# Kernel optimization log

Hardware: AMD Instinct MI355X
Metric: run time of the kernel (lower is better)

The kernel has to match this reference:

```python
import jax, jax.numpy as jnp
import numpy as np

GH, GW, H = 9, 9, 128
EPS = 1e-5


def _ln(v, g, b):
    mu = v.mean(-1, keepdims=True)
    var = ((v - mu) ** 2).mean(-1, keepdims=True)
    return (v - mu) * jax.lax.rsqrt(var + EPS) * g + b


def _bn(v, g, b):
    # BatchNorm1d in training mode: batch statistics, biased variance
    mu = v.mean(0)
    var = ((v - mu) ** 2).mean(0)
    return (v - mu) * jax.lax.rsqrt(var + EPS) * g + b


def _forward(x, h_ext, c_ext, h_grid0, c_grid0, Wh, bh, Wc, bc,
             lnh_g, lnh_b, lnc_g, lnc_b, W_ih, b_ih, W_hh, b_hh,
             fc1_W, fc1_b, bn1_g, bn1_b, fc2_W, fc2_b, bn2_g, bn2_b,
             fc3_W, fc3_b, bno_g, bno_b):
    B = x.shape[0]
    zeros = jnp.zeros((B, H), x.dtype)
    h_cur = [[None] * GW for _ in range(GH)]
    c_cur = [[None] * GW for _ in range(GH)]
    for i in range(GH):
        for j in range(GW):
            k = i * GW + j
            h_prev, c_prev = h_grid0[i, j], c_grid0[i, j]  # [B, H]
            if i == 0 and j == 0:
                h_left, c_left = h_ext, c_ext
            elif j > 0:
                h_left, c_left = h_cur[i][j - 1], c_cur[i][j - 1]
            else:
                h_left, c_left = zeros, zeros
            if i > 0:
                h_up, c_up = h_cur[i - 1][j], c_cur[i - 1][j]
            else:
                h_up, c_up = zeros, zeros
            comb_h = jnp.concatenate([h_left, h_up, h_prev], axis=1)  # [B, 3H]
            comb_c = jnp.concatenate([c_left, c_up, c_prev], axis=1)
            ph = _ln(comb_h @ Wh[k].T + bh[k], lnh_g[k], lnh_b[k])  # dropout is identity (eval)
            pc = _ln(comb_c @ Wc[k].T + bc[k], lnc_g[k], lnc_b[k])
            xin = x[:, i, j][:, None]  # [B, 1]
            gates = xin @ W_ih[k].T + b_ih[k] + ph @ W_hh[k].T + b_hh[k]  # [B, 4H]
            ig, fg, gg, og = jnp.split(gates, 4, axis=1)
            c_new = jax.nn.sigmoid(fg) * pc + jax.nn.sigmoid(ig) * jnp.tanh(gg)
            h_new = jax.nn.sigmoid(og) * jnp.tanh(c_new)
            h_cur[i][j], c_cur[i][j] = h_new, c_new
    final_h = h_cur[-1][-1] + h_ext
    final_c = c_cur[-1][-1] + c_ext
    z = jnp.concatenate([final_h, final_c], axis=1)  # [B, 2H]
    z = jax.nn.relu(_bn(z @ fc1_W.T + fc1_b, bn1_g, bn1_b))
    z = jax.nn.relu(_bn(z @ fc2_W.T + fc2_b, bn2_g, bn2_b))
    z = z @ fc3_W.T + fc3_b
    return jax.nn.sigmoid(_bn(z, bno_g, bno_b))


def setup_inputs() -> dict:
    key = jax.random.key(0)
    ks = jax.random.split(key, 16)
    B, OUT = 4096, 1
    N = GH * GW
    s = 0.05
    f32 = jnp.float32
    return {
        "x": jax.random.normal(ks[0], (B, GH, GW), f32),
        "h_ext": jax.random.normal(ks[1], (B, H), f32),
        "c_ext": jax.random.normal(ks[2], (B, H), f32),
        "h_grid0": jnp.zeros((GH, GW, B, H), f32),
        "c_grid0": jnp.zeros((GH, GW, B, H), f32),
        "Wh": jax.random.normal(ks[3], (N, H, 3 * H), f32) * s,
        "bh": jnp.zeros((N, H), f32),
        "Wc": jax.random.normal(ks[4], (N, H, 3 * H), f32) * s,
        "bc": jnp.zeros((N, H), f32),
        "lnh_g": jnp.ones((N, H), f32),
        "lnh_b": jnp.zeros((N, H), f32),
        "lnc_g": jnp.ones((N, H), f32),
        "lnc_b": jnp.zeros((N, H), f32),
        "W_ih": jax.random.normal(ks[5], (N, 4 * H, 1), f32) * s,
        "b_ih": jnp.zeros((N, 4 * H), f32),
        "W_hh": jax.random.normal(ks[6], (N, 4 * H, H), f32) * s,
        "b_hh": jnp.zeros((N, 4 * H), f32),
        "fc1_W": jax.random.normal(ks[7], (256, 2 * H), f32) * s,
        "fc1_b": jnp.zeros((256,), f32),
        "bn1_g": jnp.ones((256,), f32),
        "bn1_b": jnp.zeros((256,), f32),
        "fc2_W": jax.random.normal(ks[8], (128, 256), f32) * s,
        "fc2_b": jnp.zeros((128,), f32),
        "bn2_g": jnp.ones((128,), f32),
        "bn2_b": jnp.zeros((128,), f32),
        "fc3_W": jax.random.normal(ks[9], (OUT, 128), f32) * s,
        "fc3_b": jnp.zeros((OUT,), f32),
        "bno_g": jnp.ones((OUT,), f32),
        "bno_b": jnp.zeros((OUT,), f32),
    }


def reference(x, h_ext, c_ext, h_grid0, c_grid0, Wh, bh, Wc, bc,
              lnh_g, lnh_b, lnc_g, lnc_b, W_ih, b_ih, W_hh, b_hh,
              fc1_W, fc1_b, bn1_g, bn1_b, fc2_W, fc2_b, bn2_g, bn2_b,
              fc3_W, fc3_b, bno_g, bno_b):
    return _forward(x, h_ext, c_ext, h_grid0, c_grid0, Wh, bh, Wc, bc,
                    lnh_g, lnh_b, lnc_g, lnc_b, W_ih, b_ih, W_hh, b_hh,
                    fc1_W, fc1_b, bn1_g, bn1_b, fc2_W, fc2_b, bn2_g, bn2_b,
                    fc3_W, fc3_b, bno_g, bno_b)
```

## Files before the change

### kernel.cpp

```cpp
#include <hip/hip_runtime.h>
#include <math.h>

#define HH      128
#define GHN     9
#define GWN     9
#define BATCH   4096
#define NCELL   81
#define MSAMP   16
#define THREADS 512
#define NBLK    (BATCH / MSAMP)
#define EPSF    1e-5f

typedef __attribute__((ext_vector_type(8))) short  bf8;
typedef __attribute__((ext_vector_type(4))) short  short4v;
typedef __attribute__((ext_vector_type(4))) float  f32x4;

#define MFMA(a, b, c) __builtin_amdgcn_mfma_f32_16x16x32_bf16(a, b, c, 0, 0, 0)

__device__ __forceinline__ float rcp_fast(float x) { return __builtin_amdgcn_rcpf(x); }
__device__ __forceinline__ float rsq_fast(float x) { return __builtin_amdgcn_rsqf(x); }
__device__ __forceinline__ float sigm(float x)     { return rcp_fast(1.f + __expf(-x)); }
__device__ __forceinline__ float tanh_fast(float x) {
    float ax = fabsf(x);
    float t  = __expf(-2.f * ax);
    float r  = (1.f - t) * rcp_fast(1.f + t);
    return (x < 0.f) ? -r : r;
}
__device__ __forceinline__ short f2bf(float f) {
    unsigned u = __float_as_uint(f);
    u = (u + 0x7FFFu + ((u >> 16) & 1u)) >> 16;
    return (short)u;
}
__device__ __forceinline__ float bf2f(short h) {
    return __uint_as_float(((unsigned)(unsigned short)h) << 16);
}
__device__ __forceinline__ void split_bf(float f, short& hi, short& lo) {
    hi = f2bf(f);
    lo = f2bf(f - bf2f(hi));
}
__device__ __forceinline__ void store_frag4(short* hiA, short* loA, int idx, float4 v) {
    short4v h, l; short a, b;
    split_bf(v.x, a, b); h.x = a; l.x = b;
    split_bf(v.y, a, b); h.y = a; l.y = b;
    split_bf(v.z, a, b); h.z = a; l.z = b;
    split_bf(v.w, a, b); h.w = a; l.w = b;
    *(short4v*)&hiA[idx] = h;
    *(short4v*)&loA[idx] = l;
}
__device__ __forceinline__ int frag4_idx(int k, int m) {
    return (k >> 5) * 512 + ((((k & 31) >> 3) << 4) | m) * 8 + (k & 7);
}

__global__ __launch_bounds__(256)
void k_buildw(const float* __restrict__ Wh, const float* __restrict__ Wc,
              const float* __restrict__ Whh,
              short* __restrict__ whB_hi, short* __restrict__ whB_lo,
              short* __restrict__ wcB_hi, short* __restrict__ wcB_lo,
              short* __restrict__ whhB_hi, short* __restrict__ whhB_lo)
{
    __shared__ float lw[32 * 384];
    const int u  = threadIdx.x;
    const int kc = blockIdx.x / 24;
    const int c  = blockIdx.x % 24;

    if (c < 8) {
        const int mat = c >> 2;
        const int p   = c & 3;
        const float* src = (mat ? Wc : Wh) + ((size_t)kc * 128 + 32 * p) * 384;
        #pragma unroll
        for (int it = 0; it < 12; ++it)
            ((float4*)lw)[it * 256 + u] = ((const float4*)src)[it * 256 + u];
        __syncthreads();
        short* Dhi = mat ? wcB_hi : whB_hi;
        short* Dlo = mat ? wcB_lo : whB_lo;
        #pragma unroll
        for (int it = 0; it < 6; ++it) {
            const int wd = it * 256 + u;
            const int tt = wd / 768;
            const int rm = wd - tt * 768;
            const int s  = rm >> 6;
            const int l  = rm & 63;
            const int rl = tt * 16 + (l & 15);
            const int kk = s * 32 + (l >> 4) * 8;
            const float* pr = &lw[rl * 384 + kk];
            const float4 v0 = *(const float4*)pr;
            const float4 v1 = *(const float4*)(pr + 4);
            const size_t dst = (((size_t)kc * 8 + (2 * p + tt)) * 12 + s) * 512 + l * 8;
            short4v h, lo; short a, b;
            split_bf(v0.x, a, b); h.x = a; lo.x = b;
            split_bf(v0.y, a, b); h.y = a; lo.y = b;
            split_bf(v0.z, a, b); h.z = a; lo.z = b;
            split_bf(v0.w, a, b); h.w = a; lo.w = b;
            *(short4v*)&Dhi[dst]     = h;  *(short4v*)&Dlo[dst]     = lo;
            split_bf(v1.x, a, b); h.x = a; lo.x = b;
            split_bf(v1.y, a, b); h.y = a; lo.y = b;
            split_bf(v1.z, a, b); h.z = a; lo.z = b;
            split_bf(v1.w, a, b); h.w = a; lo.w = b;
            *(short4v*)&Dhi[dst + 4] = h;  *(short4v*)&Dlo[dst + 4] = lo;
        }
    } else {
        const int cc = c - 8;
        const float* src = Whh + ((size_t)kc * 512 + 32 * cc) * 128;
        #pragma unroll
        for (int it = 0; it < 4; ++it)
            ((float4*)lw)[it * 256 + u] = ((const float4*)src)[it * 256 + u];
        __syncthreads();
        #pragma unroll
        for (int it = 0; it < 2; ++it) {
            const int wd = it * 256 + u;
            const int tt = wd >> 8;
            const int rm = wd & 255;
            const int s  = rm >> 6;
            const int l  = rm & 63;
            const int rl = tt * 16 + (l & 15);
            const int kk = s * 32 + (l >> 4) * 8;
            const float* pr = &lw[rl * 128 + kk];
            const float4 v0 = *(const float4*)pr;
            const float4 v1 = *(const float4*)(pr + 4);
            const size_t dst = (((size_t)kc * 32 + (2 * cc + tt)) * 4 + s) * 512 + l * 8;
            short4v h, lo; short a, b;
            split_bf(v0.x, a, b); h.x = a; lo.x = b;
            split_bf(v0.y, a, b); h.y = a; lo.y = b;
            split_bf(v0.z, a, b); h.z = a; lo.z = b;
            split_bf(v0.w, a, b); h.w = a; lo.w = b;
            *(short4v*)&whhB_hi[dst]     = h;  *(short4v*)&whhB_lo[dst]     = lo;
            split_bf(v1.x, a, b); h.x = a; lo.x = b;
            split_bf(v1.y, a, b); h.y = a; lo.y = b;
            split_bf(v1.z, a, b); h.z = a; lo.z = b;
            split_bf(v1.w, a, b); h.w = a; lo.w = b;
            *(short4v*)&whhB_hi[dst + 4] = h;  *(short4v*)&whhB_lo[dst + 4] = lo;
        }
    }
}

__global__ __launch_bounds__(THREADS, 2)
void k_lattice(const float* __restrict__ x, const float* __restrict__ h_ext,
               const float* __restrict__ c_ext, const float* __restrict__ h_g0,
               const float* __restrict__ c_g0,
               const short* __restrict__ whB_hi, const short* __restrict__ whB_lo,
               const short* __restrict__ wcB_hi, const short* __restrict__ wcB_lo,
               const short* __restrict__ whhB_hi, const short* __restrict__ whhB_lo,
               const float* __restrict__ bh, const float* __restrict__ bc,
               const float* __restrict__ lnh_g, const float* __restrict__ lnh_b,
               const float* __restrict__ lnc_g, const float* __restrict__ lnc_b,
               const float* __restrict__ W_ih, const float* __restrict__ b_ih,
               const float* __restrict__ b_hh,
               float* __restrict__ hrowB, float* __restrict__ crowB,
               float* __restrict__ zout)
{
    __shared__ __align__(16) short sAH_hi[12 * 512], sAH_lo[12 * 512];
    __shared__ __align__(16) short sAC_hi[12 * 512], sAC_lo[12 * 512];
    __shared__ __align__(16) short sPh_hi[4 * 512],  sPh_lo[4 * 512];
    __shared__ float pcArr[16 * 132];
    __shared__ float part[2 * 4 * 16 * 2];
    __shared__ float xsArr[16 * NCELL];

    const int t    = threadIdx.x;
    const int base = blockIdx.x * MSAMP;
    const int lane = t & 63;
    const int w    = t >> 6;
    const int cL   = lane & 15;
    const int gL   = lane >> 4;

    const int mat = w >> 2;
    const int p   = w & 3;
    const int m_b = t >> 5;
    const int f4  = (t & 31) * 4;

    for (int idx = t; idx < MSAMP * NCELL; idx += THREADS) {
        const int m = idx / NCELL;
        const int cc = idx - m * NCELL;
        xsArr[idx] = x[(size_t)(base + m) * NCELL + cc];
    }
    const float4 z4 = make_float4(0.f, 0.f, 0.f, 0.f);

    for (int i = 0; i < GHN; ++i) {
      for (int j = 0; j < GWN; ++j) {
        const int k = i * GWN + j;

        {
            if (j == 0) {
                float4 hv = z4, cv = z4;
                if (i == 0) {
                    hv = *(const float4*)&h_ext[(size_t)(base + m_b) * HH + f4];
                    cv = *(const float4*)&c_ext[(size_t)(base + m_b) * HH + f4];
                }
                store_frag4(sAH_hi, sAH_lo, frag4_idx(f4, m_b), hv);
                store_frag4(sAC_hi, sAC_lo, frag4_idx(f4, m_b), cv);
            }
            float4 uh = z4, uc = z4;
            if (i > 0) {
                uh = *(const float4*)&hrowB[((size_t)(base + m_b) * GWN + j) * HH + f4];
                uc = *(const float4*)&crowB[((size_t)(base + m_b) * GWN + j) * HH + f4];
            }
            store_frag4(sAH_hi, sAH_lo, frag4_idx(128 + f4, m_b), uh);
            store_frag4(sAC_hi, sAC_lo, frag4_idx(128 + f4, m_b), uc);
            const float4 pv = *(const float4*)&h_g0[((size_t)k * BATCH + base + m_b) * HH + f4];
            const float4 qv = *(const float4*)&c_g0[((size_t)k * BATCH + base + m_b) * HH + f4];
            store_frag4(sAH_hi, sAH_lo, frag4_idx(256 + f4, m_b), pv);
            store_frag4(sAC_hi, sAC_lo, frag4_idx(256 + f4, m_b), qv);
        }
        __syncthreads();

        const int t0 = 2 * p, t1 = 2 * p + 1;
        const short* Ahi = mat ? sAC_hi : sAH_hi;
        const short* Alo = mat ? sAC_lo : sAH_lo;
        const short* Bhi = (mat ? wcB_hi : whB_hi) + (size_t)k * 49152;
        const short* Blo = (mat ? wcB_lo : whB_lo) + (size_t)k * 49152;
        f32x4 d0 = {0.f, 0.f, 0.f, 0.f}, d1 = {0.f, 0.f, 0.f, 0.f};
        #pragma unroll 4
        for (int ks = 0; ks < 12; ++ks) {
            const bf8 ah  = *(const bf8*)&Ahi[ks * 512 + lane * 8];
            const bf8 al  = *(const bf8*)&Alo[ks * 512 + lane * 8];
            const bf8 b0h = *(const bf8*)&Bhi[(t0 * 12 + ks) * 512 + lane * 8];
            const bf8 b0l = *(const bf8*)&Blo[(t0 * 12 + ks) * 512 + lane * 8];
            const bf8 b1h = *(const bf8*)&Bhi[(t1 * 12 + ks) * 512 + lane * 8];
            const bf8 b1l = *(const bf8*)&Blo[(t1 * 12 + ks) * 512 + lane * 8];
            d0 = MFMA(al, b0l, d0); d0 = MFMA(al, b0h, d0);
            d0 = MFMA(ah, b0l, d0); d0 = MFMA(ah, b0h, d0);
            d1 = MFMA(al, b1l, d1); d1 = MFMA(al, b1h, d1);
            d1 = MFMA(ah, b1l, d1); d1 = MFMA(ah, b1h, d1);
        }
        const int f0 = t0 * 16 + cL, f1 = t1 * 16 + cL;
        {
            const float* bias = mat ? bc : bh;
            const float bb0 = bias[k * HH + f0], bb1 = bias[k * HH + f1];
            d0 += bb0; d1 += bb1;
        }
        {
            float ps[4], pq[4];
            #pragma unroll
            for (int r = 0; r < 4; ++r) {
                ps[r] = d0[r] + d1[r];
                pq[r] = d0[r] * d0[r] + d1[r] * d1[r];
            }
            #pragma unroll
            for (int msk = 1; msk < 16; msk <<= 1) {
                #pragma unroll
                for (int r = 0; r < 4; ++r) {
                    ps[r] += __shfl_xor(ps[r], msk);
                    pq[r] += __shfl_xor(pq[r], msk);
                }
            }
            if (cL == 0) {
                #pragma unroll
                for (int r = 0; r < 4; ++r) {
                    part[((mat * 4 + p) * 16 + gL * 4 + r) * 2 + 0] = ps[r];
                    part[((mat * 4 + p) * 16 + gL * 4 + r) * 2 + 1] = pq[r];
                }
            }
        }
        __syncthreads();

        {
            const float* lng = mat ? lnc_g : lnh_g;
            const float* lnb = mat ? lnc_b : lnh_b;
            const float g0 = lng[k * HH + f0], g1 = lng[k * HH + f1];
            const float e0 = lnb[k * HH + f0], e1 = lnb[k * HH + f1];
            #pragma unroll
            for (int r = 0; r < 4; ++r) {
                const int s = gL * 4 + r;
                float ts = 0.f, tq = 0.f;
                #pragma unroll
                for (int pp = 0; pp < 4; ++pp) {
                    ts += part[((mat * 4 + pp) * 16 + s) * 2 + 0];
                    tq += part[((mat * 4 + pp) * 16 + s) * 2 + 1];
                }
                const float mu = ts * (1.f / HH);
                const float rstd = rsq_fast(tq * (1.f / HH) - mu * mu + EPSF);
                const float v0 = (d0[r] - mu) * rstd * g0 + e0;
                const float v1 = (d1[r] - mu) * rstd * g1 + e1;
                if (mat == 0) {
                    const int e0i = (f0 >> 5) * 512 + ((((f0 & 31) >> 3) << 4) | s) * 8 + (f0 & 7);
                    const int e1i = (f1 >> 5) * 512 + ((((f1 & 31) >> 3) << 4) | s) * 8 + (f1 & 7);
                    short hi, lo;
                    split_bf(v0, hi, lo); sPh_hi[e0i] = hi; sPh_lo[e0i] = lo;
                    split_bf(v1, hi, lo); sPh_hi[e1i] = hi; sPh_lo[e1i] = lo;
                } else {
                    pcArr[s * 132 + f0] = v0;
                    pcArr[s * 132 + f1] = v1;
                }
            }
        }
        __syncthreads();

        f32x4 ga0 = {0.f,0.f,0.f,0.f}, ga1 = ga0, ga2 = ga0, ga3 = ga0;
        {
            const short* GBhi = whhB_hi + (size_t)k * 65536;
            const short* GBlo = whhB_lo + (size_t)k * 65536;
            #pragma unroll
            for (int ks = 0; ks < 4; ++ks) {
                const bf8 ah = *(const bf8*)&sPh_hi[ks * 512 + lane * 8];
                const bf8 al = *(const bf8*)&sPh_lo[ks * 512 + lane * 8];
                const bf8 bh0 = *(const bf8*)&GBhi[((w     ) * 4 + ks) * 512 + lane * 8];
                const bf8 bl0 = *(const bf8*)&GBlo[((w     ) * 4 + ks) * 512 + lane * 8];
                const bf8 bh1 = *(const bf8*)&GBhi[((w +  8) * 4 + ks) * 512 + lane * 8];
                const bf8 bl1 = *(const bf8*)&GBlo[((w +  8) * 4 + ks) * 512 + lane * 8];
                const bf8 bh2 = *(const bf8*)&GBhi[((w + 16) * 4 + ks) * 512 + lane * 8];
                const bf8 bl2 = *(const bf8*)&GBlo[((w + 16) * 4 + ks) * 512 + lane * 8];
                const bf8 bh3 = *(const bf8*)&GBhi[((w + 24) * 4 + ks) * 512 + lane * 8];
                const bf8 bl3 = *(const bf8*)&GBlo[((w + 24) * 4 + ks) * 512 + lane * 8];
                ga0 = MFMA(al, bl0, ga0); ga0 = MFMA(al, bh0, ga0);
                ga0 = MFMA(ah, bl0, ga0); ga0 = MFMA(ah, bh0, ga0);
                ga1 = MFMA(al, bl1, ga1); ga1 = MFMA(al, bh1, ga1);
                ga1 = MFMA(ah, bl1, ga1); ga1 = MFMA(ah, bh1, ga1);
                ga2 = MFMA(al, bl2, ga2); ga2 = MFMA(al, bh2, ga2);
                ga2 = MFMA(ah, bl2, ga2); ga2 = MFMA(ah, bh2, ga2);
                ga3 = MFMA(al, bl3, ga3); ga3 = MFMA(al, bh3, ga3);
                ga3 = MFMA(ah, bl3, ga3); ga3 = MFMA(ah, bh3, ga3);
            }
        }
        {
            const int q0 = w * 16 + cL;
            const float wi0 = W_ih[k * 512 + q0      ];
            const float wi1 = W_ih[k * 512 + q0 + 128];
            const float wi2 = W_ih[k * 512 + q0 + 256];
            const float wi3 = W_ih[k * 512 + q0 + 384];
            const float bs0 = b_ih[k * 512 + q0      ] + b_hh[k * 512 + q0      ];
            const float bs1 = b_ih[k * 512 + q0 + 128] + b_hh[k * 512 + q0 + 128];
            const float bs2 = b_ih[k * 512 + q0 + 256] + b_hh[k * 512 + q0 + 256];
            const float bs3 = b_ih[k * 512 + q0 + 384] + b_hh[k * 512 + q0 + 384];
            #pragma unroll
            for (int r = 0; r < 4; ++r) {
                const int s = gL * 4 + r;
                const int b = base + s;
                const float xv = xsArr[s * NCELL + k];
                const float gi_ = ga0[r] + bs0 + wi0 * xv;
                const float gf_ = ga1[r] + bs1 + wi1 * xv;
                const float gg_ = ga2[r] + bs2 + wi2 * xv;
                const float go_ = ga3[r] + bs3 + wi3 * xv;
                const float pcv = pcArr[s * 132 + q0];
                const float cn = sigm(gf_) * pcv + sigm(gi_) * tanh_fast(gg_);
                const float hn = sigm(go_) * tanh_fast(cn);
                if (k == NCELL - 1) {
                    zout[(size_t)b * 256 + q0]       = hn + h_ext[(size_t)b * HH + q0];
                    zout[(size_t)b * 256 + 128 + q0] = cn + c_ext[(size_t)b * HH + q0];
                } else {
                    if (j < GWN - 1) {
                        const int ei = (q0 >> 5) * 512 + ((((q0 & 31) >> 3) << 4) | s) * 8 + (q0 & 7);
                        short hi, lo;
                        split_bf(hn, hi, lo); sAH_hi[ei] = hi; sAH_lo[ei] = lo;
                        split_bf(cn, hi, lo); sAC_hi[ei] = hi; sAC_lo[ei] = lo;
                    }
                    if (i < GHN - 1) {
                        hrowB[((size_t)b * GWN + j) * HH + q0] = hn;
                        crowB[((size_t)b * GWN + j) * HH + q0] = cn;
                    }
                }
            }
        }
      }
    }
}

__global__ __launch_bounds__(256)
void k_fc1(const float* __restrict__ z, const float* __restrict__ W,
           const float* __restrict__ bias, float* __restrict__ y1,
           float* __restrict__ s1, float* __restrict__ q1)
{
    __shared__ float at[256 * 16];
    const int t   = threadIdx.x;
    const int row = t & 15;
    const int cg  = t >> 4;
    const int rb  = blockIdx.x * 16;
    {
        const float* zr = z + (size_t)(rb + row) * 256 + cg * 16;
        #pragma unroll
        for (int v = 0; v < 4; ++v) {
            const float4 zz = *(const float4*)(zr + v * 4);
            const int kk = cg * 16 + v * 4;
            at[(kk + 0) * 16 + row] = zz.x;
            at[(kk + 1) * 16 + row] = zz.y;
            at[(kk + 2) * 16 + row] = zz.z;
            at[(kk + 3) * 16 + row] = zz.w;
        }
    }
    __syncthreads();
    const int c0 = cg * 16;
    float acc[16];
    #pragma unroll
    for (int c = 0; c < 16; ++c) acc[c] = bias[c0 + c];
    for (int kb = 0; kb < 64; ++kb) {
        const float a0 = at[(4 * kb + 0) * 16 + row];
        const float a1 = at[(4 * kb + 1) * 16 + row];
        const float a2 = at[(4 * kb + 2) * 16 + row];
        const float a3 = at[(4 * kb + 3) * 16 + row];
        #pragma unroll
        for (int c = 0; c < 16; ++c) {
            const float4 wv = *(const float4*)&W[(size_t)(c0 + c) * 256 + 4 * kb];
            acc[c] += a0 * wv.x + a1 * wv.y + a2 * wv.z + a3 * wv.w;
        }
    }
    {
        float* yr = y1 + (size_t)(rb + row) * 256 + c0;
        #pragma unroll
        for (int v = 0; v < 4; ++v)
            *(float4*)(yr + v * 4) = make_float4(acc[4*v], acc[4*v+1], acc[4*v+2], acc[4*v+3]);
    }
    #pragma unroll
    for (int c = 0; c < 16; ++c) {
        float s = acc[c], sq = acc[c] * acc[c];
        s += __shfl_xor(s, 1); sq += __shfl_xor(sq, 1);
        s += __shfl_xor(s, 2); sq += __shfl_xor(sq, 2);
        s += __shfl_xor(s, 4); sq += __shfl_xor(sq, 4);
        s += __shfl_xor(s, 8); sq += __shfl_xor(sq, 8);
        if (row == 0) { atomicAdd(&s1[c0 + c], s); atomicAdd(&q1[c0 + c], sq); }
    }
}

__global__ __launch_bounds__(256)
void k_fc2(const float* __restrict__ y1, const float* __restrict__ W,
           const float* __restrict__ bias,
           const float* __restrict__ s1, const float* __restrict__ q1,
           const float* __restrict__ g1, const float* __restrict__ b1,
           float* __restrict__ y2, float* __restrict__ s2, float* __restrict__ q2)
{
    __shared__ float at[256 * 16];
    __shared__ float scale[256], shift[256];
    const int t = threadIdx.x;
    {
        const float mu  = s1[t] * (1.f / BATCH);
        const float var = q1[t] * (1.f / BATCH) - mu * mu;
        const float sc  = g1[t] * rsq_fast(var + EPSF);
        scale[t] = sc;
        shift[t] = b1[t] - mu * sc;
    }
    __syncthreads();
    const int row = t & 15;
    const int cg  = t >> 4;
    const int rb  = blockIdx.x * 16;
    {
        const float* yr = y1 + (size_t)(rb + row) * 256 + cg * 16;
        #pragma unroll
        for (int v = 0; v < 4; ++v) {
            const float4 zz = *(const float4*)(yr + v * 4);
            const int kk = cg * 16 + v * 4;
            at[(kk + 0) * 16 + row] = fmaxf(zz.x * scale[kk + 0] + shift[kk + 0], 0.f);
            at[(kk + 1) * 16 + row] = fmaxf(zz.y * scale[kk + 1] + shift[kk + 1], 0.f);
            at[(kk + 2) * 16 + row] = fmaxf(zz.z * scale[kk + 2] + shift[kk + 2], 0.f);
            at[(kk + 3) * 16 + row] = fmaxf(zz.w * scale[kk + 3] + shift[kk + 3], 0.f);
        }
    }
    __syncthreads();
    const int c0 = cg * 8;
    float acc[8];
    #pragma unroll
    for (int c = 0; c < 8; ++c) acc[c] = bias[c0 + c];
    for (int kb = 0; kb < 64; ++kb) {
        const float a0 = at[(4 * kb + 0) * 16 + row];
        const float a1 = at[(4 * kb + 1) * 16 + row];
        const float a2 = at[(4 * kb + 2) * 16 + row];
        const float a3 = at[(4 * kb + 3) * 16 + row];
        #pragma unroll
        for (int c = 0; c < 8; ++c) {
            const float4 wv = *(const float4*)&W[(size_t)(c0 + c) * 256 + 4 * kb];
            acc[c] += a0 * wv.x + a1 * wv.y + a2 * wv.z + a3 * wv.w;
        }
    }
    {
        float* yr = y2 + (size_t)(rb + row) * 128 + c0;
        *(float4*)(yr)     = make_float4(acc[0], acc[1], acc[2], acc[3]);
        *(float4*)(yr + 4) = make_float4(acc[4], acc[5], acc[6], acc[7]);
    }
    #pragma unroll
    for (int c = 0; c < 8; ++c) {
        float s = acc[c], sq = acc[c] * acc[c];
        s += __shfl_xor(s, 1); sq += __shfl_xor(sq, 1);
        s += __shfl_xor(s, 2); sq += __shfl_xor(sq, 2);
        s += __shfl_xor(s, 4); sq += __shfl_xor(sq, 4);
        s += __shfl_xor(s, 8); sq += __shfl_xor(sq, 8);
        if (row == 0) { atomicAdd(&s2[c0 + c], s); atomicAdd(&q2[c0 + c], sq); }
    }
}

__global__ __launch_bounds__(256)
void k_fc3(const float* __restrict__ y2, const float* __restrict__ W3,
           const float* __restrict__ b3,
           const float* __restrict__ s2, const float* __restrict__ q2,
           const float* __restrict__ g2, const float* __restrict__ b2,
           float* __restrict__ y3, float* __restrict__ s3, float* __restrict__ q3)
{
    __shared__ float scale[128], shift[128], w3s[128];
    const int t = threadIdx.x;
    if (t < 128) {
        const float mu  = s2[t] * (1.f / BATCH);
        const float var = q2[t] * (1.f / BATCH) - mu * mu;
        const float sc  = g2[t] * rsq_fast(var + EPSF);
        scale[t] = sc;
        shift[t] = b2[t] - mu * sc;
        w3s[t]   = W3[t];
    }
    __syncthreads();
    const int r = blockIdx.x * 256 + t;
    float acc = b3[0];
    const float* yr = y2 + (size_t)r * 128;
    for (int kb = 0; kb < 32; ++kb) {
        const float4 v = *(const float4*)(yr + 4 * kb);
        const int kk = 4 * kb;
        acc += fmaxf(v.x * scale[kk + 0] + shift[kk + 0], 0.f) * w3s[kk + 0];
        acc += fmaxf(v.y * scale[kk + 1] + shift[kk + 1], 0.f) * w3s[kk + 1];
        acc += fmaxf(v.z * scale[kk + 2] + shift[kk + 2], 0.f) * w3s[kk + 2];
        acc += fmaxf(v.w * scale[kk + 3] + shift[kk + 3], 0.f) * w3s[kk + 3];
    }
// ... 88 lines not shown
```

Baseline: 1.902 ms.

## Double lattice block to 1024 threads and drop low-by-low MFMA term

Doubles the threads per block so each of 16 waves computes one 16-column tile of the projection GEMMs instead of two, and splits the staging loads between the h and c halves of the block. It drops the lo*lo product in the split-bf16 three-term emulation for both the projection and gate GEMMs, cutting MFMA count by a quarter at a small precision cost. Only half the waves run the gate GEMM and LSTM update, so those waves idle during that phase, and the launch bound asks for 4 blocks per CU, which constrains registers.

```diff
diff --git a/kernel.cpp b/kernel.cpp
--- a/kernel.cpp
+++ b/kernel.cpp
@@ -7,7 +7,7 @@
 #define BATCH   4096
 #define NCELL   81
 #define MSAMP   16
-#define THREADS 512
+#define THREADS 1024
 #define NBLK    (BATCH / MSAMP)
 #define EPSF    1e-5f
 
@@ -133,7 +133,7 @@
     }
 }
 
-__global__ __launch_bounds__(THREADS, 2)
+__global__ __launch_bounds__(THREADS, 4)
 void k_lattice(const float* __restrict__ x, const float* __restrict__ h_ext,
                const float* __restrict__ c_ext, const float* __restrict__ h_g0,
                const float* __restrict__ c_g0,
@@ -152,7 +152,7 @@
     __shared__ __align__(16) short sAC_hi[12 * 512], sAC_lo[12 * 512];
     __shared__ __align__(16) short sPh_hi[4 * 512],  sPh_lo[4 * 512];
     __shared__ float pcArr[16 * 132];
-    __shared__ float part[2 * 4 * 16 * 2];
+    __shared__ float part_s[2 * 8 * 16], part_q[2 * 8 * 16];
     __shared__ float xsArr[16 * NCELL];
 
     const int t    = threadIdx.x;
@@ -162,10 +162,14 @@
     const int cL   = lane & 15;
     const int gL   = lane >> 4;
 
-    const int mat = w >> 2;
-    const int p   = w & 3;
-    const int m_b = t >> 5;
-    const int f4  = (t & 31) * 4;
+    const int mat = w >> 3;
+    const int tt  = w & 7;
+    const int f0  = tt * 16 + cL;
+    const int q0  = w * 16 + cL;
+    const int mat_b = t >> 9;
+    const int tb    = t & 511;
+    const int m_b   = tb >> 5;
+    const int f4    = (tb & 31) * 4;
 
     for (int idx = t; idx < MSAMP * NCELL; idx += THREADS) {
         const int m = idx / NCELL;
@@ -174,66 +178,54 @@
     }
     const float4 z4 = make_float4(0.f, 0.f, 0.f, 0.f);
 
+    #pragma unroll 1
     for (int i = 0; i < GHN; ++i) {
+      #pragma unroll 1
       for (int j = 0; j < GWN; ++j) {
         const int k = i * GWN + j;
 
         {
+            short* Dhi = mat_b ? sAC_hi : sAH_hi;
+            short* Dlo = mat_b ? sAC_lo : sAH_lo;
+            const float* extp = mat_b ? c_ext : h_ext;
+            const float* rowp = mat_b ? crowB : hrowB;
+            const float* g0p  = mat_b ? c_g0  : h_g0;
             if (j == 0) {
-                float4 hv = z4, cv = z4;
-                if (i == 0) {
-                    hv = *(const float4*)&h_ext[(size_t)(base + m_b) * HH + f4];
-                    cv = *(const float4*)&c_ext[(size_t)(base + m_b) * HH + f4];
-                }
-                store_frag4(sAH_hi, sAH_lo, frag4_idx(f4, m_b), hv);
-                store_frag4(sAC_hi, sAC_lo, frag4_idx(f4, m_b), cv);
+                float4 v = z4;
+                if (i == 0) v = *(const float4*)&extp[(size_t)(base + m_b) * HH + f4];
+                store_frag4(Dhi, Dlo, frag4_idx(f4, m_b), v);
             }
-            float4 uh = z4, uc = z4;
-            if (i > 0) {
-                uh = *(const float4*)&hrowB[((size_t)(base + m_b) * GWN + j) * HH + f4];
-                uc = *(const float4*)&crowB[((size_t)(base + m_b) * GWN + j) * HH + f4];
-            }
-            store_frag4(sAH_hi, sAH_lo, frag4_idx(128 + f4, m_b), uh);
-            store_frag4(sAC_hi, sAC_lo, frag4_idx(128 + f4, m_b), uc);
-            const float4 pv = *(const float4*)&h_g0[((size_t)k * BATCH + base + m_b) * HH + f4];
-            const float4 qv = *(const float4*)&c_g0[((size_t)k * BATCH + base + m_b) * HH + f4];
-            store_frag4(sAH_hi, sAH_lo, frag4_idx(256 + f4, m_b), pv);
-            store_frag4(sAC_hi, sAC_lo, frag4_idx(256 + f4, m_b), qv);
+            float4 uv = z4;
+            if (i > 0) uv = *(const float4*)&rowp[((size_t)(base + m_b) * GWN + j) * HH + f4];
+            store_frag4(Dhi, Dlo, frag4_idx(128 + f4, m_b), uv);
+            const float4 pv = *(const float4*)&g0p[((size_t)k * BATCH + base + m_b) * HH + f4];
+            store_frag4(Dhi, Dlo, frag4_idx(256 + f4, m_b), pv);
         }
         __syncthreads();
 
-        const int t0 = 2 * p, t1 = 2 * p + 1;
         const short* Ahi = mat ? sAC_hi : sAH_hi;
         const short* Alo = mat ? sAC_lo : sAH_lo;
         const short* Bhi = (mat ? wcB_hi : whB_hi) + (size_t)k * 49152;
         const short* Blo = (mat ? wcB_lo : whB_lo) + (size_t)k * 49152;
-        f32x4 d0 = {0.f, 0.f, 0.f, 0.f}, d1 = {0.f, 0.f, 0.f, 0.f};
+        f32x4 d0 = {0.f, 0.f, 0.f, 0.f};
         #pragma unroll 4
         for (int ks = 0; ks < 12; ++ks) {
-            const bf8 ah  = *(const bf8*)&Ahi[ks * 512 + lane * 8];
-            const bf8 al  = *(const bf8*)&Alo[ks * 512 + lane * 8];
-            const bf8 b0h = *(const bf8*)&Bhi[(t0 * 12 + ks) * 512 + lane * 8];
-            const bf8 b0l = *(const bf8*)&Blo[(t0 * 12 + ks) * 512 + lane * 8];
-            const bf8 b1h = *(const bf8*)&Bhi[(t1 * 12 + ks) * 512 + lane * 8];
-            const bf8 b1l = *(const bf8*)&Blo[(t1 * 12 + ks) * 512 + lane * 8];
-            d0 = MFMA(al, b0l, d0); d0 = MFMA(al, b0h, d0);
-            d0 = MFMA(ah, b0l, d0); d0 = MFMA(ah, b0h, d0);
-            d1 = MFMA(al, b1l, d1); d1 = MFMA(al, b1h, d1);
-            d1 = MFMA(ah, b1l, d1); d1 = MFMA(ah, b1h, d1);
-        }
-        const int f0 = t0 * 16 + cL, f1 = t1 * 16 + cL;
+            const bf8 ah = *(const bf8*)&Ahi[ks * 512 + lane * 8];
+            const bf8 al = *(const bf8*)&Alo[ks * 512 + lane * 8];
+            const bf8 bh_ = *(const bf8*)&Bhi[(tt * 12 + ks) * 512 + lane * 8];
+            const bf8 bl_ = *(const bf8*)&Blo[(tt * 12 + ks) * 512 + lane * 8];
+            d0 = MFMA(al, bh_, d0);
+            d0 = MFMA(ah, bl_, d0);
+            d0 = MFMA(ah, bh_, d0);
+        }
         {
             const float* bias = mat ? bc : bh;
-            const float bb0 = bias[k * HH + f0], bb1 = bias[k * HH + f1];
-            d0 += bb0; d1 += bb1;
+            d0 += bias[k * HH + f0];
         }
         {
             float ps[4], pq[4];
             #pragma unroll
-            for (int r = 0; r < 4; ++r) {
-                ps[r] = d0[r] + d1[r];
-                pq[r] = d0[r] * d0[r] + d1[r] * d1[r];
-            }
+            for (int r = 0; r < 4; ++r) { ps[r] = d0[r]; pq[r] = d0[r] * d0[r]; }
             #pragma unroll
             for (int msk = 1; msk < 16; msk <<= 1) {
                 #pragma unroll
@@ -245,8 +237,8 @@
             if (cL == 0) {
                 #pragma unroll
                 for (int r = 0; r < 4; ++r) {
-                    part[((mat * 4 + p) * 16 + gL * 4 + r) * 2 + 0] = ps[r];
-                    part[((mat * 4 + p) * 16 + gL * 4 + r) * 2 + 1] = pq[r];
+                    part_s[(mat * 8 + tt) * 16 + gL * 4 + r] = ps[r];
+                    part_q[(mat * 8 + tt) * 16 + gL * 4 + r] = pq[r];
                 }
             }
         }
@@ -255,96 +247,89 @@
         {
             const float* lng = mat ? lnc_g : lnh_g;
             const float* lnb = mat ? lnc_b : lnh_b;
-            const float g0 = lng[k * HH + f0], g1 = lng[k * HH + f1];
-            const float e0 = lnb[k * HH + f0], e1 = lnb[k * HH + f1];
+            const float g0 = lng[k * HH + f0];
+            const float e0 = lnb[k * HH + f0];
             #pragma unroll
             for (int r = 0; r < 4; ++r) {
                 const int s = gL * 4 + r;
                 float ts = 0.f, tq = 0.f;
                 #pragma unroll
-                for (int pp = 0; pp < 4; ++pp) {
-                    ts += part[((mat * 4 + pp) * 16 + s) * 2 + 0];
-                    tq += part[((mat * 4 + pp) * 16 + s) * 2 + 1];
+                for (int pp = 0; pp < 8; ++pp) {
+                    ts += part_s[(mat * 8 + pp) * 16 + s];
+                    tq += part_q[(mat * 8 + pp) * 16 + s];
                 }
                 const float mu = ts * (1.f / HH);
                 const float rstd = rsq_fast(tq * (1.f / HH) - mu * mu + EPSF);
                 const float v0 = (d0[r] - mu) * rstd * g0 + e0;
-                const float v1 = (d1[r] - mu) * rstd * g1 + e1;
                 if (mat == 0) {
                     const int e0i = (f0 >> 5) * 512 + ((((f0 & 31) >> 3) << 4) | s) * 8 + (f0 & 7);
-                    const int e1i = (f1 >> 5) * 512 + ((((f1 & 31) >> 3) << 4) | s) * 8 + (f1 & 7);
                     short hi, lo;
                     split_bf(v0, hi, lo); sPh_hi[e0i] = hi; sPh_lo[e0i] = lo;
-                    split_bf(v1, hi, lo); sPh_hi[e1i] = hi; sPh_lo[e1i] = lo;
                 } else {
                     pcArr[s * 132 + f0] = v0;
-                    pcArr[s * 132 + f1] = v1;
                 }
             }
         }
         __syncthreads();
 
-        f32x4 ga0 = {0.f,0.f,0.f,0.f}, ga1 = ga0, ga2 = ga0, ga3 = ga0;
-        {
-            const short* GBhi = whhB_hi + (size_t)k * 65536;
-            const short* GBlo = whhB_lo + (size_t)k * 65536;
-            #pragma unroll
-            for (int ks = 0; ks < 4; ++ks) {
-                const bf8 ah = *(const bf8*)&sPh_hi[ks * 512 + lane * 8];
-                const bf8 al = *(const bf8*)&sPh_lo[ks * 512 + lane * 8];
-                const bf8 bh0 = *(const bf8*)&GBhi[((w     ) * 4 + ks) * 512 + lane * 8];
-                const bf8 bl0 = *(const bf8*)&GBlo[((w     ) * 4 + ks) * 512 + lane * 8];
-                const bf8 bh1 = *(const bf8*)&GBhi[((w +  8) * 4 + ks) * 512 + lane * 8];
-                const bf8 bl1 = *(const bf8*)&GBlo[((w +  8) * 4 + ks) * 512 + lane * 8];
-                const bf8 bh2 = *(const bf8*)&GBhi[((w + 16) * 4 + ks) * 512 + lane * 8];
-                const bf8 bl2 = *(const bf8*)&GBlo[((w + 16) * 4 + ks) * 512 + lane * 8];
-                const bf8 bh3 = *(const bf8*)&GBhi[((w + 24) * 4 + ks) * 512 + lane * 8];
-                const bf8 bl3 = *(const bf8*)&GBlo[((w + 24) * 4 + ks) * 512 + lane * 8];
-                ga0 = MFMA(al, bl0, ga0); ga0 = MFMA(al, bh0, ga0);
-                ga0 = MFMA(ah, bl0, ga0); ga0 = MFMA(ah, bh0, ga0);
-                ga1 = MFMA(al, bl1, ga1); ga1 = MFMA(al, bh1, ga1);
-                ga1 = MFMA(ah, bl1, ga1); ga1 = MFMA(ah, bh1, ga1);
-                ga2 = MFMA(al, bl2, ga2); ga2 = MFMA(al, bh2, ga2);
-                ga2 = MFMA(ah, bl2, ga2); ga2 = MFMA(ah, bh2, ga2);
-                ga3 = MFMA(al, bl3, ga3); ga3 = MFMA(al, bh3, ga3);
-                ga3 = MFMA(ah, bl3, ga3); ga3 = MFMA(ah, bh3, ga3);
+        if (w < 8) {
+            f32x4 ga0 = {0.f,0.f,0.f,0.f}, ga1 = ga0, ga2 = ga0, ga3 = ga0;
+            {
+                const short* GBhi = whhB_hi + (size_t)k * 65536;
+                const short* GBlo = whhB_lo + (size_t)k * 65536;
+                #pragma unroll
+                for (int ks = 0; ks < 4; ++ks) {
+                    const bf8 ah = *(const bf8*)&sPh_hi[ks * 512 + lane * 8];
+                    const bf8 al = *(const bf8*)&sPh_lo[ks * 512 + lane * 8];
+                    const bf8 bh0 = *(const bf8*)&GBhi[((w     ) * 4 + ks) * 512 + lane * 8];
+                    const bf8 bl0 = *(const bf8*)&GBlo[((w     ) * 4 + ks) * 512 + lane * 8];
+                    const bf8 bh1 = *(const bf8*)&GBhi[((w +  8) * 4 + ks) * 512 + lane * 8];
+                    const bf8 bl1 = *(const bf8*)&GBlo[((w +  8) * 4 + ks) * 512 + lane * 8];
+                    const bf8 bh2 = *(const bf8*)&GBhi[((w + 16) * 4 + ks) * 512 + lane * 8];
+                    const bf8 bl2 = *(const bf8*)&GBlo[((w + 16) * 4 + ks) * 512 + lane * 8];
+                    const bf8 bh3 = *(const bf8*)&GBhi[((w + 24) * 4 + ks) * 512 + lane * 8];
+                    const bf8 bl3 = *(const bf8*)&GBlo[((w + 24) * 4 + ks) * 512 + lane * 8];
+                    ga0 = MFMA(al, bh0, ga0); ga0 = MFMA(ah, bl0, ga0); ga0 = MFMA(ah, bh0, ga0);
+                    ga1 = MFMA(al, bh1, ga1); ga1 = MFMA(ah, bl1, ga1); ga1 = MFMA(ah, bh1, ga1);
+                    ga2 = MFMA(al, bh2, ga2); ga2 = MFMA(ah, bl2, ga2); ga2 = MFMA(ah, bh2, ga2);
+                    ga3 = MFMA(al, bh3, ga3); ga3 = MFMA(ah, bl3, ga3); ga3 = MFMA(ah, bh3, ga3);
+                }
             }
-        }
-        {
-            const int q0 = w * 16 + cL;
-            const float wi0 = W_ih[k * 512 + q0      ];
-            const float wi1 = W_ih[k * 512 + q0 + 128];
-            const float wi2 = W_ih[k * 512 + q0 + 256];
-            const float wi3 = W_ih[k * 512 + q0 + 384];
-            const float bs0 = b_ih[k * 512 + q0      ] + b_hh[k * 512 + q0      ];
-            const float bs1 = b_ih[k * 512 + q0 + 128] + b_hh[k * 512 + q0 + 128];
-            const float bs2 = b_ih[k * 512 + q0 + 256] + b_hh[k * 512 + q0 + 256];
-            const float bs3 = b_ih[k * 512 + q0 + 384] + b_hh[k * 512 + q0 + 384];
-            #pragma unroll
-            for (int r = 0; r < 4; ++r) {
-                const int s = gL * 4 + r;
-                const int b = base + s;
-                const float xv = xsArr[s * NCELL + k];
-                const float gi_ = ga0[r] + bs0 + wi0 * xv;
-                const float gf_ = ga1[r] + bs1 + wi1 * xv;
-                const float gg_ = ga2[r] + bs2 + wi2 * xv;
-                const float go_ = ga3[r] + bs3 + wi3 * xv;
-                const float pcv = pcArr[s * 132 + q0];
-                const float cn = sigm(gf_) * pcv + sigm(gi_) * tanh_fast(gg_);
-                const float hn = sigm(go_) * tanh_fast(cn);
-                if (k == NCELL - 1) {
-                    zout[(size_t)b * 256 + q0]       = hn + h_ext[(size_t)b * HH + q0];
-                    zout[(size_t)b * 256 + 128 + q0] = cn + c_ext[(size_t)b * HH + q0];
-                } else {
-                    if (j < GWN - 1) {
-                        const int ei = (q0 >> 5) * 512 + ((((q0 & 31) >> 3) << 4) | s) * 8 + (q0 & 7);
-                        short hi, lo;
-                        split_bf(hn, hi, lo); sAH_hi[ei] = hi; sAH_lo[ei] = lo;
-                        split_bf(cn, hi, lo); sAC_hi[ei] = hi; sAC_lo[ei] = lo;
-                    }
-                    if (i < GHN - 1) {
-                        hrowB[((size_t)b * GWN + j) * HH + q0] = hn;
-                        crowB[((size_t)b * GWN + j) * HH + q0] = cn;
+            {
+                const float wi0 = W_ih[k * 512 + q0      ];
+                const float wi1 = W_ih[k * 512 + q0 + 128];
+                const float wi2 = W_ih[k * 512 + q0 + 256];
+                const float wi3 = W_ih[k * 512 + q0 + 384];
+                const float bs0 = b_ih[k * 512 + q0      ] + b_hh[k * 512 + q0      ];
+                const float bs1 = b_ih[k * 512 + q0 + 128] + b_hh[k * 512 + q0 + 128];
+                const float bs2 = b_ih[k * 512 + q0 + 256] + b_hh[k * 512 + q0 + 256];
+                const float bs3 = b_ih[k * 512 + q0 + 384] + b_hh[k * 512 + q0 + 384];
+                #pragma unroll
+                for (int r = 0; r < 4; ++r) {
+                    const int s = gL * 4 + r;
+                    const int b = base + s;
+                    const float xv = xsArr[s * NCELL + k];
+                    const float gi_ = ga0[r] + bs0 + wi0 * xv;
+                    const float gf_ = ga1[r] + bs1 + wi1 * xv;
+                    const float gg_ = ga2[r] + bs2 + wi2 * xv;
+                    const float go_ = ga3[r] + bs3 + wi3 * xv;
+                    const float pcv = pcArr[s * 132 + q0];
+                    const float cn = sigm(gf_) * pcv + sigm(gi_) * tanh_fast(gg_);
+                    const float hn = sigm(go_) * tanh_fast(cn);
+                    if (k == NCELL - 1) {
+                        zout[(size_t)b * 256 + q0]       = hn + h_ext[(size_t)b * HH + q0];
+                        zout[(size_t)b * 256 + 128 + q0] = cn + c_ext[(size_t)b * HH + q0];
+                    } else {
+                        if (j < GWN - 1) {
+                            const int ei = (q0 >> 5) * 512 + ((((q0 & 31) >> 3) << 4) | s) * 8 + (q0 & 7);
+                            short hi, lo;
+                            split_bf(hn, hi, lo); sAH_hi[ei] = hi; sAH_lo[ei] = lo;
+                            split_bf(cn, hi, lo); sAC_hi[ei] = hi; sAC_lo[ei] = lo;
+                        }
+                        if (i < GHN - 1) {
+                            hrowB[((size_t)b * GWN + j) * HH + q0] = hn;
+                            crowB[((size_t)b * GWN + j) * HH + q0] = cn;
+                        }
                     }
                 }
             }
```

Result: slower. 2.153 ms (+13.2%).

## Restructure lattice cell step: prefetch next inputs, drop barrier, 3-term bf16 split

Applied to the files above, without the earlier changes.

The per-cell loop now prefetches the next cell's row and initial-state inputs into registers and issues the first weight-fragment loads before the barrier. It also removes one of the three block barriers by writing raw projections to shared memory and applying LayerNorm inside the gate GEMM and the cell update. The error-compensated bf16 GEMMs drop the lo×lo MFMA term, going from 4 to 3 MFMAs per fragment, and the wave-to-matrix mapping is reassigned. This cuts barrier and global-load latency and MFMA count, at the cost of more registers, redundant LN normalisation work, and slightly lower precision.

```diff
diff --git a/kernel.cpp b/kernel.cpp
--- a/kernel.cpp
+++ b/kernel.cpp
@@ -49,6 +49,11 @@
 }
 __device__ __forceinline__ int frag4_idx(int k, int m) {
     return (k >> 5) * 512 + ((((k & 31) >> 3) << 4) | m) * 8 + (k & 7);
+}
+__device__ __forceinline__ void barrier_lgkm() {
+    asm volatile("s_waitcnt lgkmcnt(0)" ::: "memory");
+    __builtin_amdgcn_s_barrier();
+    __builtin_amdgcn_sched_barrier(0);
 }
 
 __global__ __launch_bounds__(256)
@@ -150,9 +155,8 @@
 {
     __shared__ __align__(16) short sAH_hi[12 * 512], sAH_lo[12 * 512];
     __shared__ __align__(16) short sAC_hi[12 * 512], sAC_lo[12 * 512];
-    __shared__ __align__(16) short sPh_hi[4 * 512],  sPh_lo[4 * 512];
-    __shared__ float pcArr[16 * 132];
-    __shared__ float part[2 * 4 * 16 * 2];
+    __shared__ float phRaw[16 * 132], pcRaw[16 * 132];
+    __shared__ float part_s[16 * 16], part_q[16 * 16];
     __shared__ float xsArr[16 * NCELL];
 
     const int t    = threadIdx.x;
@@ -162,8 +166,11 @@
     const int cL   = lane & 15;
     const int gL   = lane >> 4;
 
-    const int mat = w >> 2;
-    const int p   = w & 3;
+    const int mat = w & 1;
+    const int tp  = w >> 1;
+    const int t0  = tp, t1 = tp + 4;
+    const int f0  = t0 * 16 + cL, f1 = t1 * 16 + cL;
+    const int q0  = w * 16 + cL;
     const int m_b = t >> 5;
     const int f4  = (t & 31) * 4;
 
@@ -173,145 +180,187 @@
         xsArr[idx] = x[(size_t)(base + m) * NCELL + cc];
     }
     const float4 z4 = make_float4(0.f, 0.f, 0.f, 0.f);
-
+    float4 pfUH = z4, pfUC = z4, pfPH = z4, pfPC = z4;
+    bool havePf = false;
+
+    #pragma unroll 1
     for (int i = 0; i < GHN; ++i) {
+      #pragma unroll 1
       for (int j = 0; j < GWN; ++j) {
         const int k = i * GWN + j;
 
         {
+            float4 uh, uc, pv, qv;
+            if (havePf) { uh = pfUH; uc = pfUC; pv = pfPH; qv = pfPC; }
+            else {
+                if (i > 0) {
+                    uh = *(const float4*)&hrowB[((size_t)(base + m_b) * GWN + j) * HH + f4];
+                    uc = *(const float4*)&crowB[((size_t)(base + m_b) * GWN + j) * HH + f4];
+                } else { uh = z4; uc = z4; }
+                pv = *(const float4*)&h_g0[((size_t)k * BATCH + base + m_b) * HH + f4];
+                qv = *(const float4*)&c_g0[((size_t)k * BATCH + base + m_b) * HH + f4];
+            }
             if (j == 0) {
-                float4 hv = z4, cv = z4;
+                float4 lh = z4, lc = z4;
                 if (i == 0) {
-                    hv = *(const float4*)&h_ext[(size_t)(base + m_b) * HH + f4];
-                    cv = *(const float4*)&c_ext[(size_t)(base + m_b) * HH + f4];
+                    lh = *(const float4*)&h_ext[(size_t)(base + m_b) * HH + f4];
+                    lc = *(const float4*)&c_ext[(size_t)(base + m_b) * HH + f4];
                 }
-                store_frag4(sAH_hi, sAH_lo, frag4_idx(f4, m_b), hv);
-                store_frag4(sAC_hi, sAC_lo, frag4_idx(f4, m_b), cv);
-            }
-            float4 uh = z4, uc = z4;
-            if (i > 0) {
-                uh = *(const float4*)&hrowB[((size_t)(base + m_b) * GWN + j) * HH + f4];
-                uc = *(const float4*)&crowB[((size_t)(base + m_b) * GWN + j) * HH + f4];
+                store_frag4(sAH_hi, sAH_lo, frag4_idx(f4, m_b), lh);
+                store_frag4(sAC_hi, sAC_lo, frag4_idx(f4, m_b), lc);
             }
             store_frag4(sAH_hi, sAH_lo, frag4_idx(128 + f4, m_b), uh);
             store_frag4(sAC_hi, sAC_lo, frag4_idx(128 + f4, m_b), uc);
-            const float4 pv = *(const float4*)&h_g0[((size_t)k * BATCH + base + m_b) * HH + f4];
-            const float4 qv = *(const float4*)&c_g0[((size_t)k * BATCH + base + m_b) * HH + f4];
             store_frag4(sAH_hi, sAH_lo, frag4_idx(256 + f4, m_b), pv);
             store_frag4(sAC_hi, sAC_lo, frag4_idx(256 + f4, m_b), qv);
-        }
-        __syncthreads();
-
-        const int t0 = 2 * p, t1 = 2 * p + 1;
+
+            if (j < GWN - 1) {
+                if (i > 0) {
+                    pfUH = *(const float4*)&hrowB[((size_t)(base + m_b) * GWN + j + 1) * HH + f4];
+                    pfUC = *(const float4*)&crowB[((size_t)(base + m_b) * GWN + j + 1) * HH + f4];
+                } else { pfUH = z4; pfUC = z4; }
+                pfPH = *(const float4*)&h_g0[((size_t)(k + 1) * BATCH + base + m_b) * HH + f4];
+                pfPC = *(const float4*)&c_g0[((size_t)(k + 1) * BATCH + base + m_b) * HH + f4];
+                havePf = true;
+            } else havePf = false;
+        }
+
         const short* Ahi = mat ? sAC_hi : sAH_hi;
         const short* Alo = mat ? sAC_lo : sAH_lo;
         const short* Bhi = (mat ? wcB_hi : whB_hi) + (size_t)k * 49152;
         const short* Blo = (mat ? wcB_lo : whB_lo) + (size_t)k * 49152;
+        const bf8 hw0h = *(const bf8*)&Bhi[(t0 * 12) * 512 + lane * 8];
+        const bf8 hw0l = *(const bf8*)&Blo[(t0 * 12) * 512 + lane * 8];
+        const bf8 hw1h = *(const bf8*)&Bhi[(t1 * 12) * 512 + lane * 8];
+        const bf8 hw1l = *(const bf8*)&Blo[(t1 * 12) * 512 + lane * 8];
+
+        barrier_lgkm();
+
         f32x4 d0 = {0.f, 0.f, 0.f, 0.f}, d1 = {0.f, 0.f, 0.f, 0.f};
+        {
+            const bf8 ah = *(const bf8*)&Ahi[lane * 8];
+            const bf8 al = *(const bf8*)&Alo[lane * 8];
+            d0 = MFMA(al, hw0h, d0); d0 = MFMA(ah, hw0l, d0); d0 = MFMA(ah, hw0h, d0);
+            d1 = MFMA(al, hw1h, d1); d1 = MFMA(ah, hw1l, d1); d1 = MFMA(ah, hw1h, d1);
+        }
         #pragma unroll 4
-        for (int ks = 0; ks < 12; ++ks) {
+        for (int ks = 1; ks < 12; ++ks) {
             const bf8 ah  = *(const bf8*)&Ahi[ks * 512 + lane * 8];
             const bf8 al  = *(const bf8*)&Alo[ks * 512 + lane * 8];
             const bf8 b0h = *(const bf8*)&Bhi[(t0 * 12 + ks) * 512 + lane * 8];
             const bf8 b0l = *(const bf8*)&Blo[(t0 * 12 + ks) * 512 + lane * 8];
             const bf8 b1h = *(const bf8*)&Bhi[(t1 * 12 + ks) * 512 + lane * 8];
             const bf8 b1l = *(const bf8*)&Blo[(t1 * 12 + ks) * 512 + lane * 8];
-            d0 = MFMA(al, b0l, d0); d0 = MFMA(al, b0h, d0);
-            d0 = MFMA(ah, b0l, d0); d0 = MFMA(ah, b0h, d0);
-            d1 = MFMA(al, b1l, d1); d1 = MFMA(al, b1h, d1);
-            d1 = MFMA(ah, b1l, d1); d1 = MFMA(ah, b1h, d1);
-        }
-        const int f0 = t0 * 16 + cL, f1 = t1 * 16 + cL;
+            d0 = MFMA(al, b0h, d0); d0 = MFMA(ah, b0l, d0); d0 = MFMA(ah, b0h, d0);
+            d1 = MFMA(al, b1h, d1); d1 = MFMA(ah, b1l, d1); d1 = MFMA(ah, b1h, d1);
+        }
         {
             const float* bias = mat ? bc : bh;
-            const float bb0 = bias[k * HH + f0], bb1 = bias[k * HH + f1];
-            d0 += bb0; d1 += bb1;
+            d0 += bias[k * HH + f0];
+            d1 += bias[k * HH + f1];
         }
         {
-            float ps[4], pq[4];
+            float ps0[4], pq0[4], ps1[4], pq1[4];
             #pragma unroll
             for (int r = 0; r < 4; ++r) {
-                ps[r] = d0[r] + d1[r];
-                pq[r] = d0[r] * d0[r] + d1[r] * d1[r];
+                ps0[r] = d0[r]; pq0[r] = d0[r] * d0[r];
+                ps1[r] = d1[r]; pq1[r] = d1[r] * d1[r];
             }
             #pragma unroll
             for (int msk = 1; msk < 16; msk <<= 1) {
                 #pragma unroll
                 for (int r = 0; r < 4; ++r) {
-                    ps[r] += __shfl_xor(ps[r], msk);
-                    pq[r] += __shfl_xor(pq[r], msk);
+                    ps0[r] += __shfl_xor(ps0[r], msk);
+                    pq0[r] += __shfl_xor(pq0[r], msk);
+                    ps1[r] += __shfl_xor(ps1[r], msk);
+                    pq1[r] += __shfl_xor(pq1[r], msk);
                 }
             }
             if (cL == 0) {
                 #pragma unroll
                 for (int r = 0; r < 4; ++r) {
-                    part[((mat * 4 + p) * 16 + gL * 4 + r) * 2 + 0] = ps[r];
-                    part[((mat * 4 + p) * 16 + gL * 4 + r) * 2 + 1] = pq[r];
+                    const int s = gL * 4 + r;
+                    part_s[(mat * 8 + t0) * 16 + s] = ps0[r];
+                    part_q[(mat * 8 + t0) * 16 + s] = pq0[r];
+                    part_s[(mat * 8 + t1) * 16 + s] = ps1[r];
+                    part_q[(mat * 8 + t1) * 16 + s] = pq1[r];
                 }
             }
-        }
-        __syncthreads();
-
-        {
-            const float* lng = mat ? lnc_g : lnh_g;
-            const float* lnb = mat ? lnc_b : lnh_b;
-            const float g0 = lng[k * HH + f0], g1 = lng[k * HH + f1];
-            const float e0 = lnb[k * HH + f0], e1 = lnb[k * HH + f1];
+            float* RW = mat ? pcRaw : phRaw;
             #pragma unroll
             for (int r = 0; r < 4; ++r) {
                 const int s = gL * 4 + r;
-                float ts = 0.f, tq = 0.f;
-                #pragma unroll
-                for (int pp = 0; pp < 4; ++pp) {
-                    ts += part[((mat * 4 + pp) * 16 + s) * 2 + 0];
-                    tq += part[((mat * 4 + pp) * 16 + s) * 2 + 1];
-                }
-                const float mu = ts * (1.f / HH);
-                const float rstd = rsq_fast(tq * (1.f / HH) - mu * mu + EPSF);
-                const float v0 = (d0[r] - mu) * rstd * g0 + e0;
-                const float v1 = (d1[r] - mu) * rstd * g1 + e1;
-                if (mat == 0) {
-                    const int e0i = (f0 >> 5) * 512 + ((((f0 & 31) >> 3) << 4) | s) * 8 + (f0 & 7);
-                    const int e1i = (f1 >> 5) * 512 + ((((f1 & 31) >> 3) << 4) | s) * 8 + (f1 & 7);
-                    short hi, lo;
-                    split_bf(v0, hi, lo); sPh_hi[e0i] = hi; sPh_lo[e0i] = lo;
-                    split_bf(v1, hi, lo); sPh_hi[e1i] = hi; sPh_lo[e1i] = lo;
-                } else {
-                    pcArr[s * 132 + f0] = v0;
-                    pcArr[s * 132 + f1] = v1;
-                }
-            }
-        }
-        __syncthreads();
+                RW[s * 132 + f0] = d0[r];
+                RW[s * 132 + f1] = d1[r];
+            }
+        }
+
+        const short* GBhi = whhB_hi + (size_t)k * 65536;
+        const short* GBlo = whhB_lo + (size_t)k * 65536;
+        const bf8 gw0h = *(const bf8*)&GBhi[((w     ) * 4) * 512 + lane * 8];
+        const bf8 gw0l = *(const bf8*)&GBlo[((w     ) * 4) * 512 + lane * 8];
+        const bf8 gw1h = *(const bf8*)&GBhi[((w +  8) * 4) * 512 + lane * 8];
+        const bf8 gw1l = *(const bf8*)&GBlo[((w +  8) * 4) * 512 + lane * 8];
+        const bf8 gw2h = *(const bf8*)&GBhi[((w + 16) * 4) * 512 + lane * 8];
+        const bf8 gw2l = *(const bf8*)&GBlo[((w + 16) * 4) * 512 + lane * 8];
+        const bf8 gw3h = *(const bf8*)&GBhi[((w + 24) * 4) * 512 + lane * 8];
+        const bf8 gw3l = *(const bf8*)&GBlo[((w + 24) * 4) * 512 + lane * 8];
+
+        barrier_lgkm();
 
         f32x4 ga0 = {0.f,0.f,0.f,0.f}, ga1 = ga0, ga2 = ga0, ga3 = ga0;
+        float muH, rsH;
         {
-            const short* GBhi = whhB_hi + (size_t)k * 65536;
-            const short* GBlo = whhB_lo + (size_t)k * 65536;
+            float ts = 0.f, tq = 0.f;
             #pragma unroll
-            for (int ks = 0; ks < 4; ++ks) {
-                const bf8 ah = *(const bf8*)&sPh_hi[ks * 512 + lane * 8];
-                const bf8 al = *(const bf8*)&sPh_lo[ks * 512 + lane * 8];
-                const bf8 bh0 = *(const bf8*)&GBhi[((w     ) * 4 + ks) * 512 + lane * 8];
-                const bf8 bl0 = *(const bf8*)&GBlo[((w     ) * 4 + ks) * 512 + lane * 8];
-                const bf8 bh1 = *(const bf8*)&GBhi[((w +  8) * 4 + ks) * 512 + lane * 8];
-                const bf8 bl1 = *(const bf8*)&GBlo[((w +  8) * 4 + ks) * 512 + lane * 8];
-                const bf8 bh2 = *(const bf8*)&GBhi[((w + 16) * 4 + ks) * 512 + lane * 8];
-                const bf8 bl2 = *(const bf8*)&GBlo[((w + 16) * 4 + ks) * 512 + lane * 8];
-                const bf8 bh3 = *(const bf8*)&GBhi[((w + 24) * 4 + ks) * 512 + lane * 8];
-                const bf8 bl3 = *(const bf8*)&GBlo[((w + 24) * 4 + ks) * 512 + lane * 8];
-                ga0 = MFMA(al, bl0, ga0); ga0 = MFMA(al, bh0, ga0);
-                ga0 = MFMA(ah, bl0, ga0); ga0 = MFMA(ah, bh0, ga0);
-                ga1 = MFMA(al, bl1, ga1); ga1 = MFMA(al, bh1, ga1);
-                ga1 = MFMA(ah, bl1, ga1); ga1 = MFMA(ah, bh1, ga1);
-                ga2 = MFMA(al, bl2, ga2); ga2 = MFMA(al, bh2, ga2);
-                ga2 = MFMA(ah, bl2, ga2); ga2 = MFMA(ah, bh2, ga2);
-                ga3 = MFMA(al, bl3, ga3); ga3 = MFMA(al, bh3, ga3);
-                ga3 = MFMA(ah, bl3, ga3); ga3 = MFMA(ah, bh3, ga3);
-            }
-        }
+            for (int pp = 0; pp < 8; ++pp) { ts += part_s[pp * 16 + cL]; tq += part_q[pp * 16 + cL]; }
+            muH = ts * (1.f / HH);
+            rsH = rsq_fast(tq * (1.f / HH) - muH * muH + EPSF);
+        }
+        #pragma unroll
+        for (int ks = 0; ks < 4; ++ks) {
+            const float* pr = &phRaw[cL * 132 + ks * 32 + gL * 8];
+            const float4 va = *(const float4*)pr;
+            const float4 vb = *(const float4*)(pr + 4);
+            const int fb = k * HH + ks * 32 + gL * 8;
+            const float4 lg0 = *(const float4*)&lnh_g[fb];
+            const float4 lg1 = *(const float4*)&lnh_g[fb + 4];
+            const float4 lb0 = *(const float4*)&lnh_b[fb];
+            const float4 lb1 = *(const float4*)&lnh_b[fb + 4];
+            bf8 ah, al;
+            {
+                short hi, lo; float vv;
+                vv = (va.x - muH) * rsH * lg0.x + lb0.x; split_bf(vv, hi, lo); ah[0] = hi; al[0] = lo;
+                vv = (va.y - muH) * rsH * lg0.y + lb0.y; split_bf(vv, hi, lo); ah[1] = hi; al[1] = lo;
+                vv = (va.z - muH) * rsH * lg0.z + lb0.z; split_bf(vv, hi, lo); ah[2] = hi; al[2] = lo;
+                vv = (va.w - muH) * rsH * lg0.w + lb0.w; split_bf(vv, hi, lo); ah[3] = hi; al[3] = lo;
+                vv = (vb.x - muH) * rsH * lg1.x + lb1.x; split_bf(vv, hi, lo); ah[4] = hi; al[4] = lo;
+                vv = (vb.y - muH) * rsH * lg1.y + lb1.y; split_bf(vv, hi, lo); ah[5] = hi; al[5] = lo;
+                vv = (vb.z - muH) * rsH * lg1.z + lb1.z; split_bf(vv, hi, lo); ah[6] = hi; al[6] = lo;
+                vv = (vb.w - muH) * rsH * lg1.w + lb1.w; split_bf(vv, hi, lo); ah[7] = hi; al[7] = lo;
+            }
+            bf8 b0h, b0l, b1h, b1l, b2h, b2l, b3h, b3l;
+            if (ks == 0) {
+                b0h = gw0h; b0l = gw0l; b1h = gw1h; b1l = gw1l;
+                b2h = gw2h; b2l = gw2l; b3h = gw3h; b3l = gw3l;
+            } else {
+                b0h = *(const bf8*)&GBhi[((w     ) * 4 + ks) * 512 + lane * 8];
+                b0l = *(const bf8*)&GBlo[((w     ) * 4 + ks) * 512 + lane * 8];
+                b1h = *(const bf8*)&GBhi[((w +  8) * 4 + ks) * 512 + lane * 8];
+                b1l = *(const bf8*)&GBlo[((w +  8) * 4 + ks) * 512 + lane * 8];
+                b2h = *(const bf8*)&GBhi[((w + 16) * 4 + ks) * 512 + lane * 8];
+                b2l = *(const bf8*)&GBlo[((w + 16) * 4 + ks) * 512 + lane * 8];
+                b3h = *(const bf8*)&GBhi[((w + 24) * 4 + ks) * 512 + lane * 8];
+                b3l = *(const bf8*)&GBlo[((w + 24) * 4 + ks) * 512 + lane * 8];
+            }
+            ga0 = MFMA(al, b0h, ga0); ga0 = MFMA(ah, b0l, ga0); ga0 = MFMA(ah, b0h, ga0);
+            ga1 = MFMA(al, b1h, ga1); ga1 = MFMA(ah, b1l, ga1); ga1 = MFMA(ah, b1h, ga1);
+            ga2 = MFMA(al, b2h, ga2); ga2 = MFMA(ah, b2l, ga2); ga2 = MFMA(ah, b2h, ga2);
+            ga3 = MFMA(al, b3h, ga3); ga3 = MFMA(ah, b3l, ga3); ga3 = MFMA(ah, b3h, ga3);
+        }
+
         {
-            const int q0 = w * 16 + cL;
+            const float gcq = lnc_g[k * HH + q0], ecq = lnc_b[k * HH + q0];
             const float wi0 = W_ih[k * 512 + q0      ];
             const float wi1 = W_ih[k * 512 + q0 + 128];
             const float wi2 = W_ih[k * 512 + q0 + 256];
@@ -324,12 +373,17 @@
             for (int r = 0; r < 4; ++r) {
                 const int s = gL * 4 + r;
                 const int b = base + s;
-                const float xv = xsArr[s * NCELL + k];
+                float ts = 0.f, tq = 0.f;
+                #pragma unroll
+                for (int pp = 8; pp < 16; ++pp) { ts += part_s[pp * 16 + s]; tq += part_q[pp * 16 + s]; }
+                const float muC = ts * (1.f / HH);
+                const float rsC = rsq_fast(tq * (1.f / HH) - muC * muC + EPSF);
+                const float pcv = (pcRaw[s * 132 + q0] - muC) * rsC * gcq + ecq;
+                const float xv  = xsArr[s * NCELL + k];
                 const float gi_ = ga0[r] + bs0 + wi0 * xv;
                 const float gf_ = ga1[r] + bs1 + wi1 * xv;
                 const float gg_ = ga2[r] + bs2 + wi2 * xv;
                 const float go_ = ga3[r] + bs3 + wi3 * xv;
-                const float pcv = pcArr[s * 132 + q0];
                 const float cn = sigm(gf_) * pcv + sigm(gi_) * tanh_fast(gg_);
                 const float hn = sigm(go_) * tanh_fast(cn);
                 if (k == NCELL - 1) {
@@ -349,6 +403,7 @@
                 }
             }
         }
+        if (j == GWN - 1) asm volatile("s_waitcnt vmcnt(0)" ::: "memory");
       }
     }
 }
```

After: 2.644 ms. 1.39x slower.
